# Performance work log

Hardware: AMD Instinct MI355X
Metric: run time of the kernel (lower is better)

Reference implementation:

```python
import jax, jax.numpy as jnp
import numpy as np

N, E = 40000, 640000          # nodes, edges (avg degree 16)
IN_N, IN_E = 8 + 768, 2       # in_dim_node + in_dim_text, in_dim_edge
H, OUT, NC, L = 128, 128, 5, 2
EPS_BN, EPS_DEN = 1e-5, 1e-6


def setup_inputs() -> dict:
    key = jax.random.key(0)
    ks = jax.random.split(key, 16)
    w = lambda k, shape: jax.random.normal(k, shape, jnp.float32) * 0.05
    return {
        "node_feat": jax.random.normal(ks[0], (N, IN_N), jnp.float32),
        "edge_feat": jax.random.normal(ks[1], (E, IN_E), jnp.float32),
        "src": jax.random.randint(ks[2], (E,), 0, N),
        "dst": jax.random.randint(ks[3], (E,), 0, N),
        "enc_nw": w(ks[4], (IN_N, H)), "enc_nb": jnp.zeros((H,), jnp.float32),
        "enc_ew": w(ks[5], (IN_E, H)), "enc_eb": jnp.zeros((H,), jnp.float32),
        # per layer: 5 linears (order A, B, C, D, E)
        "lin_w": w(ks[6], (L, 5, H, H)), "lin_b": jnp.zeros((L, 5, H), jnp.float32),
        "bnh_g": jnp.ones((L, H), jnp.float32), "bnh_b": jnp.zeros((L, H), jnp.float32),
        "bne_g": jnp.ones((L, H), jnp.float32), "bne_b": jnp.zeros((L, H), jnp.float32),
        "mlp_w1": w(ks[7], (H, OUT)), "mlp_b1": jnp.zeros((OUT,), jnp.float32),
        "mlp_w2": w(ks[8], (OUT, NC)), "mlp_b2": jnp.zeros((NC,), jnp.float32),
    }


def _bn(x, g, b):
    # training-mode BatchNorm1d: batch stats, biased variance, eps=1e-5
    m = jnp.mean(x, axis=0)
    v = jnp.var(x, axis=0)
    return (x - m) * jax.lax.rsqrt(v + EPS_BN) * g + b


def reference(node_feat, edge_feat, src, dst, enc_nw, enc_nb, enc_ew, enc_eb,
              lin_w, lin_b, bnh_g, bnh_b, bne_g, bne_b,
              mlp_w1, mlp_b1, mlp_w2, mlp_b2):
    n = node_feat.shape[0]
    h = node_feat @ enc_nw + enc_nb          # [N, H]
    e = edge_feat @ enc_ew + enc_eb          # [E, H]
    for l in range(L):
        Ah = h @ lin_w[l, 0] + lin_b[l, 0]
        Bh = h @ lin_w[l, 1] + lin_b[l, 1]
        Ce = e @ lin_w[l, 2] + lin_b[l, 2]
        Dh = h @ lin_w[l, 3] + lin_b[l, 3]
        Eh = h @ lin_w[l, 4] + lin_b[l, 4]
        e_new = Ce + Dh[src] + Eh[dst]       # [E, H] edge gate logits
        sigma = jax.nn.sigmoid(e_new)
        num = jax.ops.segment_sum(sigma * Bh[src], dst, num_segments=n)
        den = jax.ops.segment_sum(sigma, dst, num_segments=n)
        h_new = Ah + num / (den + EPS_DEN)
        h = jax.nn.relu(_bn(h_new, bnh_g[l], bnh_b[l]))
        e = jax.nn.relu(_bn(e_new, bne_g[l], bne_b[l]))
    # MLP readout per node (dropout p=0 -> identity)
    logits = jax.nn.relu(h @ mlp_w1 + mlp_b1) @ mlp_w2 + mlp_b2
    return logits
```

## Files before the change

kernel.cpp:

```cpp
#include <hip/hip_runtime.h>
#include <math.h>

#define NN 40000
#define NE 640000
#define KIN 776
#define HH 128
#define NCLS 5

typedef __attribute__((ext_vector_type(8))) short bf16x8;
typedef __attribute__((ext_vector_type(4))) short bf16x4;
typedef __attribute__((ext_vector_type(4))) float f32x4;

__device__ __forceinline__ float bf2f(short u) {
    return __uint_as_float(((unsigned)(unsigned short)u) << 16);
}
__device__ __forceinline__ short f2bf(float f) {
    unsigned u = __float_as_uint(f);
    u += 0x7fffu + ((u >> 16) & 1u);
    return (short)(u >> 16);
}

enum { A_F32 = 0 };

template<int NSTEP, bool TAIL8>
__global__ __launch_bounds__(256)
void mfma_gemm(const float* __restrict__ Af, const short* __restrict__ Wp,
               const float* __restrict__ bias, short* __restrict__ Cb, int K)
{
    const int lane = threadIdx.x & 63;
    const int wave = threadIdx.x >> 6;
    const int q = lane >> 4;
    const int c16 = lane & 15;
    const int row = blockIdx.x * 64 + wave * 16 + c16;

    f32x4 acc[8];
#pragma unroll
    for (int n = 0; n < 8; ++n) acc[n] = (f32x4){0.f, 0.f, 0.f, 0.f};

    for (int kt = 0; kt < NSTEP; ++kt) {
        bf16x8 afrag;
        const int kbase = kt * 32 + q * 8;
        if (!TAIL8 || kt < NSTEP - 1 || q == 0) {
            const float* p = Af + (size_t)row * K + kbase;
            const float4 x = *(const float4*)p;
            const float4 y = *(const float4*)(p + 4);
            afrag[0] = f2bf(x.x); afrag[1] = f2bf(x.y);
            afrag[2] = f2bf(x.z); afrag[3] = f2bf(x.w);
            afrag[4] = f2bf(y.x); afrag[5] = f2bf(y.y);
            afrag[6] = f2bf(y.z); afrag[7] = f2bf(y.w);
        } else {
#pragma unroll
            for (int j = 0; j < 8; ++j) afrag[j] = 0;
        }
        const int kb = kt * 4 + q;
#pragma unroll
        for (int n = 0; n < 8; ++n) {
            const bf16x8 wfrag =
                *(const bf16x8*)(Wp + (size_t)kb * 1024 + (n * 16 + c16) * 8);
            acc[n] = __builtin_amdgcn_mfma_f32_16x16x32_bf16(wfrag, afrag, acc[n], 0, 0, 0);
        }
    }
#pragma unroll
    for (int n = 0; n < 8; ++n) {
        const int col = n * 16 + q * 4;
        const float4 b4 = *(const float4*)(bias + col);
        bf16x4 o;
        o[0] = f2bf(acc[n][0] + b4.x); o[1] = f2bf(acc[n][1] + b4.y);
        o[2] = f2bf(acc[n][2] + b4.z); o[3] = f2bf(acc[n][3] + b4.w);
        *(bf16x4*)(Cb + (size_t)row * HH + col) = o;
    }
}

__global__ __launch_bounds__(256)
void edge2_k(short* __restrict__ enew, const short* __restrict__ Wp,
             const float* __restrict__ bias, const float* __restrict__ bnp,
             const short* __restrict__ Dh, const short* __restrict__ Eh,
             const int* __restrict__ src_s, const int* __restrict__ dst_s)
{
    const int lane = threadIdx.x & 63;
    const int wave = threadIdx.x >> 6;
    const int q = lane >> 4;
    const int c16 = lane & 15;
    const int row0 = blockIdx.x * 128 + wave * 16 + c16;
    const int row1 = row0 + 64;

    const int s0 = src_s[row0], d0 = dst_s[row0];
    const int s1 = src_s[row1], d1 = dst_s[row1];

    f32x4 acc[2][8];
#pragma unroll
    for (int n = 0; n < 8; ++n) {
        const int col = n * 16 + q * 4;
        const float4 b4 = *(const float4*)(bias + col);
        const bf16x4 dh0 = *(const bf16x4*)(Dh + (size_t)s0 * HH + col);
        const bf16x4 eh0 = *(const bf16x4*)(Eh + (size_t)d0 * HH + col);
        const bf16x4 dh1 = *(const bf16x4*)(Dh + (size_t)s1 * HH + col);
        const bf16x4 eh1 = *(const bf16x4*)(Eh + (size_t)d1 * HH + col);
        const float bb[4] = {b4.x, b4.y, b4.z, b4.w};
#pragma unroll
        for (int j = 0; j < 4; ++j) {
            acc[0][n][j] = bb[j] + bf2f(dh0[j]) + bf2f(eh0[j]);
            acc[1][n][j] = bb[j] + bf2f(dh1[j]) + bf2f(eh1[j]);
        }
    }

#pragma unroll
    for (int kt = 0; kt < 4; ++kt) {
        const int kbase = kt * 32 + q * 8;
        const float4 sc0 = *(const float4*)(bnp + kbase);
        const float4 sc1 = *(const float4*)(bnp + kbase + 4);
        const float4 sh0 = *(const float4*)(bnp + HH + kbase);
        const float4 sh1 = *(const float4*)(bnp + HH + kbase + 4);
        const float scv[8] = {sc0.x, sc0.y, sc0.z, sc0.w, sc1.x, sc1.y, sc1.z, sc1.w};
        const float shv[8] = {sh0.x, sh0.y, sh0.z, sh0.w, sh1.x, sh1.y, sh1.z, sh1.w};
        const bf16x8 r0 = *(const bf16x8*)(enew + (size_t)row0 * HH + kbase);
        const bf16x8 r1 = *(const bf16x8*)(enew + (size_t)row1 * HH + kbase);
        bf16x8 a0, a1;
#pragma unroll
        for (int j = 0; j < 8; ++j) {
            a0[j] = f2bf(fmaxf(fmaf(bf2f(r0[j]), scv[j], shv[j]), 0.f));
            a1[j] = f2bf(fmaxf(fmaf(bf2f(r1[j]), scv[j], shv[j]), 0.f));
        }
        const int kb = kt * 4 + q;
#pragma unroll
        for (int n = 0; n < 8; ++n) {
            const bf16x8 wfrag =
                *(const bf16x8*)(Wp + (size_t)kb * 1024 + (n * 16 + c16) * 8);
            acc[0][n] = __builtin_amdgcn_mfma_f32_16x16x32_bf16(wfrag, a0, acc[0][n], 0, 0, 0);
            acc[1][n] = __builtin_amdgcn_mfma_f32_16x16x32_bf16(wfrag, a1, acc[1][n], 0, 0, 0);
        }
    }

#pragma unroll
    for (int n = 0; n < 8; ++n) {
        const int col = n * 16 + q * 4;
        bf16x4 o0, o1;
#pragma unroll
        for (int j = 0; j < 4; ++j) {
            o0[j] = f2bf(acc[0][n][j]);
            o1[j] = f2bf(acc[1][n][j]);
        }
        *(bf16x4*)(enew + (size_t)row0 * HH + col) = o0;
        *(bf16x4*)(enew + (size_t)row1 * HH + col) = o1;
    }
}

template<bool ABN>
__global__ __launch_bounds__(256, 2)
void fused4_k(const short* __restrict__ hb, const float* __restrict__ hf,
              const float* __restrict__ bnp,
              const short* __restrict__ w0, const short* __restrict__ w1,
              const short* __restrict__ w2, const short* __restrict__ w3,
              const float* __restrict__ b0, const float* __restrict__ b1,
              const float* __restrict__ b2, const float* __restrict__ b3,
              float* __restrict__ Ah, short* __restrict__ Bh,
              short* __restrict__ Dh, short* __restrict__ Eh)
{
    const int lane = threadIdx.x & 63;
    const int wave = threadIdx.x >> 6;
    const int q = lane >> 4;
    const int c16 = lane & 15;
    const int row = blockIdx.x * 64 + wave * 16 + c16;

    f32x4 acc[4][8];
#pragma unroll
    for (int t = 0; t < 4; ++t)
#pragma unroll
        for (int n = 0; n < 8; ++n) acc[t][n] = (f32x4){0.f, 0.f, 0.f, 0.f};

    const short* const ws[4] = {w0, w1, w2, w3};
#pragma unroll
    for (int kt = 0; kt < 4; ++kt) {
        const int kbase = kt * 32 + q * 8;
        bf16x8 afrag;
        if (!ABN) {
            afrag = *(const bf16x8*)(hb + (size_t)row * HH + kbase);
        } else {
            const float* p = hf + (size_t)row * HH + kbase;
            const float4 x = *(const float4*)p;
            const float4 y = *(const float4*)(p + 4);
            const float4 s0 = *(const float4*)(bnp + kbase);
            const float4 s1 = *(const float4*)(bnp + kbase + 4);
            const float4 t0 = *(const float4*)(bnp + HH + kbase);
            const float4 t1 = *(const float4*)(bnp + HH + kbase + 4);
            const float xv[8] = {x.x, x.y, x.z, x.w, y.x, y.y, y.z, y.w};
            const float scv[8] = {s0.x, s0.y, s0.z, s0.w, s1.x, s1.y, s1.z, s1.w};
            const float shv[8] = {t0.x, t0.y, t0.z, t0.w, t1.x, t1.y, t1.z, t1.w};
#pragma unroll
            for (int j = 0; j < 8; ++j)
                afrag[j] = f2bf(fmaxf(fmaf(xv[j], scv[j], shv[j]), 0.f));
        }
        const int kb = kt * 4 + q;
#pragma unroll
        for (int t = 0; t < 4; ++t)
#pragma unroll
            for (int n = 0; n < 8; ++n) {
                const bf16x8 wfrag =
                    *(const bf16x8*)(ws[t] + (size_t)kb * 1024 + (n * 16 + c16) * 8);
                acc[t][n] = __builtin_amdgcn_mfma_f32_16x16x32_bf16(wfrag, afrag, acc[t][n], 0, 0, 0);
            }
    }

    const float* const bs[4] = {b0, b1, b2, b3};
#pragma unroll
    for (int t = 0; t < 4; ++t) {
#pragma unroll
        for (int n = 0; n < 8; ++n) {
            const int col = n * 16 + q * 4;
            const float4 b4 = *(const float4*)(bs[t] + col);
            const float v[4] = {acc[t][n][0] + b4.x, acc[t][n][1] + b4.y,
                                acc[t][n][2] + b4.z, acc[t][n][3] + b4.w};
            if (t == 0) {
                *(float4*)(Ah + (size_t)row * HH + col) = make_float4(v[0], v[1], v[2], v[3]);
            } else {
                bf16x4 o;
#pragma unroll
                for (int j = 0; j < 4; ++j) o[j] = f2bf(v[j]);
                short* dstp = (t == 1) ? Bh : ((t == 2) ? Dh : Eh);
                *(bf16x4*)(dstp + (size_t)row * HH + col) = o;
            }
        }
    }
}

__global__ __launch_bounds__(256)
void readout_k(const float* __restrict__ hnew, const float* __restrict__ bnp,
               const short* __restrict__ Wp, const float* __restrict__ b1,
               const float* __restrict__ w2, const float* __restrict__ b2,
               float* __restrict__ out)
{
    const int lane = threadIdx.x & 63;
    const int wave = threadIdx.x >> 6;
    const int q = lane >> 4;
    const int c16 = lane & 15;
    const int row = blockIdx.x * 64 + wave * 16 + c16;

    f32x4 acc[8];
#pragma unroll
    for (int n = 0; n < 8; ++n) acc[n] = (f32x4){0.f, 0.f, 0.f, 0.f};

#pragma unroll
    for (int kt = 0; kt < 4; ++kt) {
        const int kbase = kt * 32 + q * 8;
        const float* p = hnew + (size_t)row * HH + kbase;
        const float4 x = *(const float4*)p;
        const float4 y = *(const float4*)(p + 4);
        const float4 s0 = *(const float4*)(bnp + kbase);
        const float4 s1 = *(const float4*)(bnp + kbase + 4);
        const float4 t0 = *(const float4*)(bnp + HH + kbase);
        const float4 t1 = *(const float4*)(bnp + HH + kbase + 4);
        const float xv[8] = {x.x, x.y, x.z, x.w, y.x, y.y, y.z, y.w};
        const float scv[8] = {s0.x, s0.y, s0.z, s0.w, s1.x, s1.y, s1.z, s1.w};
        const float shv[8] = {t0.x, t0.y, t0.z, t0.w, t1.x, t1.y, t1.z, t1.w};
        bf16x8 afrag;
#pragma unroll
        for (int j = 0; j < 8; ++j)
            afrag[j] = f2bf(fmaxf(fmaf(xv[j], scv[j], shv[j]), 0.f));
        const int kb = kt * 4 + q;
#pragma unroll
        for (int n = 0; n < 8; ++n) {
            const bf16x8 wfrag =
                *(const bf16x8*)(Wp + (size_t)kb * 1024 + (n * 16 + c16) * 8);
            acc[n] = __builtin_amdgcn_mfma_f32_16x16x32_bf16(wfrag, afrag, acc[n], 0, 0, 0);
        }
    }

    float part[NCLS] = {};
#pragma unroll
    for (int n = 0; n < 8; ++n) {
        const int col = n * 16 + q * 4;
        const float4 b4 = *(const float4*)(b1 + col);
        const float bb[4] = {b4.x, b4.y, b4.z, b4.w};
#pragma unroll
        for (int j = 0; j < 4; ++j) {
            const float zv = fmaxf(acc[n][j] + bb[j], 0.f);
#pragma unroll
            for (int t = 0; t < NCLS; ++t)
                part[t] = fmaf(zv, w2[(col + j) * NCLS + t], part[t]);
        }
    }
#pragma unroll
    for (int t = 0; t < NCLS; ++t) {
        part[t] += __shfl_xor(part[t], 16, 64);
        part[t] += __shfl_xor(part[t], 32, 64);
    }
    if (q == 0) {
#pragma unroll
        for (int t = 0; t < NCLS; ++t)
            out[(size_t)row * NCLS + t] = part[t] + b2[t];
    }
}

__global__ __launch_bounds__(256)
void prepack_k(const float* __restrict__ enc_nw, const float* __restrict__ lin_w,
               const float* __restrict__ mlp_w1, short* __restrict__ wp)
{
    const int t = blockIdx.x * 256 + threadIdx.x;
    if (t >= 260 * 128) return;
    const int kbg = t >> 7, col = t & 127;
    const int kb0[11]  = {0, 100, 116, 132, 148, 164, 180, 196, 212, 228, 244};
    const int psel[11] = {0, 1, 1, 1, 1, 1, 1, 1, 1, 1, 2};
    const int soff[11] = {0, 0 * 16384, 1 * 16384, 3 * 16384, 4 * 16384,
                          5 * 16384, 6 * 16384, 7 * 16384, 8 * 16384, 9 * 16384, 0};
    const int Ksrc[11] = {KIN, 128, 128, 128, 128, 128, 128, 128, 128, 128, 128};
    int e = 10;
    while (e > 0 && kbg < kb0[e]) --e;
    const float* base = (psel[e] == 0) ? enc_nw : ((psel[e] == 1) ? lin_w : mlp_w1);
    const int kbl = kbg - kb0[e];
    bf16x8 o;
#pragma unroll
    for (int j = 0; j < 8; ++j) {
        const int k = kbl * 8 + j;
        const float v = (k < Ksrc[e]) ? base[(size_t)soff[e] + (size_t)k * HH + col] : 0.f;
        o[j] = f2bf(v);
    }
    *(bf16x8*)(wp + (size_t)kbg * 1024 + col * 8) = o;
}

__global__ void gpre_k(const float* __restrict__ enc_ew, const float* __restrict__ enc_eb,
                       const float* __restrict__ Wc, const float* __restrict__ bc,
                       float* __restrict__ G)
{
    const int c = threadIdx.x;
    float a0 = 0.f, a1 = 0.f, ab = 0.f;
    for (int k = 0; k < HH; ++k) {
        const float w = Wc[k * HH + c];
        a0 = fmaf(enc_ew[k], w, a0);
        a1 = fmaf(enc_ew[HH + k], w, a1);
        ab = fmaf(enc_eb[k], w, ab);
    }
    G[c] = a0; G[HH + c] = a1; G[2 * HH + c] = ab + bc[c];
}

__global__ __launch_bounds__(256)
void edge1_k(const float* __restrict__ ef, const int* __restrict__ eidx,
             const int* __restrict__ src_s, const int* __restrict__ dst_s,
             const float* __restrict__ G,
             const short* __restrict__ Dh, const short* __restrict__ Eh,
             short* __restrict__ enew, float* __restrict__ pbuf)
{
    const int tid = threadIdx.x;
    const int er = tid >> 4, cg = tid & 15;
    const int col = cg * 8;
    const float4 g00 = *(const float4*)(G + col);
    const float4 g01 = *(const float4*)(G + col + 4);
    const float4 g10 = *(const float4*)(G + HH + col);
    const float4 g11 = *(const float4*)(G + HH + col + 4);
    const float4 gb0 = *(const float4*)(G + 2 * HH + col);
    const float4 gb1 = *(const float4*)(G + 2 * HH + col + 4);
    const float G0v[8] = {g00.x, g00.y, g00.z, g00.w, g01.x, g01.y, g01.z, g01.w};
    const float G1v[8] = {g10.x, g10.y, g10.z, g10.w, g11.x, g11.y, g11.z, g11.w};
    const float GBv[8] = {gb0.x, gb0.y, gb0.z, gb0.w, gb1.x, gb1.y, gb1.z, gb1.w};
    float sa[8] = {}, qa[8] = {};
    for (int it = 0; it < 16; ++it) {
        const int i = blockIdx.x * 256 + it * 16 + er;
        const int e = eidx[i];
        const float f0 = ef[(size_t)e * 2];
        const float f1 = ef[(size_t)e * 2 + 1];
        const int s = src_s[i], d = dst_s[i];
        const bf16x8 dh = *(const bf16x8*)(Dh + (size_t)s * HH + col);
        const bf16x8 eh = *(const bf16x8*)(Eh + (size_t)d * HH + col);
        bf16x8 o;
#pragma unroll
        for (int j = 0; j < 8; ++j) {
            const float v = fmaf(f0, G0v[j], fmaf(f1, G1v[j], GBv[j]))
                            + bf2f(dh[j]) + bf2f(eh[j]);
            sa[j] += v; qa[j] += v * v;
            o[j] = f2bf(v);
        }
        *(bf16x8*)(enew + (size_t)i * HH + col) = o;
    }
    __shared__ float sred[16][136];
    const int slot = (blockIdx.x & 63) * 256;
#pragma unroll
    for (int j = 0; j < 8; ++j) sred[er][col + j] = sa[j];
    __syncthreads();
    for (int s2 = 8; s2 > 0; s2 >>= 1) {
        if (er < s2)
#pragma unroll
            for (int j = 0; j < 8; ++j) sred[er][col + j] += sred[er + s2][col + j];
        __syncthreads();
    }
    if (er == 0)
#pragma unroll
        for (int j = 0; j < 8; ++j) atomicAdd(pbuf + slot + col + j, sred[0][col + j]);
    __syncthreads();
#pragma unroll
    for (int j = 0; j < 8; ++j) sred[er][col + j] = qa[j];
    __syncthreads();
    for (int s2 = 8; s2 > 0; s2 >>= 1) {
        if (er < s2)
#pragma unroll
            for (int j = 0; j < 8; ++j) sred[er][col + j] += sred[er + s2][col + j];
        __syncthreads();
    }
    if (er == 0)
#pragma unroll
        for (int j = 0; j < 8; ++j) atomicAdd(pbuf + slot + 128 + col + j, sred[0][col + j]);
}

__global__ __launch_bounds__(256)
void hist_k(const int* __restrict__ dst, int* __restrict__ cnt)
{
    const int e = blockIdx.x * 256 + threadIdx.x;
    if (e < NE) atomicAdd(cnt + dst[e], 1);
}

__global__ __launch_bounds__(1024)
void scan_k(const int* __restrict__ cnt, int* __restrict__ rowptr, int* __restrict__ wr)
{
    __shared__ int s[1024];
    const int t = threadIdx.x;
    const int base = t * 40;
    int sum = 0;
    for (int i = 0; i < 40; ++i) {
        const int idx = base + i;
        if (idx < NN) sum += cnt[idx];
    }
    s[t] = sum;
    __syncthreads();
    for (int off = 1; off < 1024; off <<= 1) {
        const int v = (t >= off) ? s[t - off] : 0;
        __syncthreads();
        s[t] += v;
        __syncthreads();
    }
    int run = (t == 0) ? 0 : s[t - 1];
    for (int i = 0; i < 40; ++i) {
        const int idx = base + i;
        if (idx < NN) {
            rowptr[idx] = run;
            wr[idx] = run;
            run += cnt[idx];
        }
    }
    if (t == 1023) rowptr[NN] = s[1023];
}

__global__ __launch_bounds__(256)
void scatter_k2(const int* __restrict__ dst, const int* __restrict__ src,
                int* __restrict__ wr, int* __restrict__ eidx,
                int* __restrict__ src_s, int* __restrict__ dst_s)
{
    const int e = blockIdx.x * 256 + threadIdx.x;
    if (e < NE) {
        const int d = dst[e];
        const int p = atomicAdd(wr + d, 1);
        eidx[p] = e;
        src_s[p] = src[e];
        dst_s[p] = d;
    }
}

__global__ __launch_bounds__(256)
void seg_reduce_v(const short* __restrict__ enew, const int* __restrict__ rowptr,
                  const int* __restrict__ src_s, const short* __restrict__ Bh,
                  const float* __restrict__ Ah, float* __restrict__ hnew,
                  float* __restrict__ pbuf)
{
    const int wv = threadIdx.x >> 6;
    const int lane = threadIdx.x & 63;
    const int slot = lane >> 4;
    const int cg = lane & 15;
    const int col = cg * 8;
    const int n0 = (blockIdx.x * 4 + wv) * 8;
    float sa[8] = {}, qa[8] = {};
    for (int nn = 0; nn < 8; ++nn) {
        const int n = n0 + nn;
        const int k0 = rowptr[n], k1 = rowptr[n + 1];
        float num[8] = {}, den[8] = {};
        for (int k = k0 + slot; k < k1; k += 4) {
            const bf16x8 ev = *(const bf16x8*)(enew + (size_t)k * HH + col);
            const int s = src_s[k];
            const bf16x8 bv = *(const bf16x8*)(Bh + (size_t)s * HH + col);
#pragma unroll
            for (int j = 0; j < 8; ++j) {
                const float sg = 1.f / (1.f + __expf(-bf2f(ev[j])));
                den[j] += sg;
                num[j] = fmaf(sg, bf2f(bv[j]), num[j]);
            }
        }
#pragma unroll
        for (int j = 0; j < 8; ++j) {
            num[j] += __shfl_xor(num[j], 16, 64);
            den[j] += __shfl_xor(den[j], 16, 64);
            num[j] += __shfl_xor(num[j], 32, 64);
            den[j] += __shfl_xor(den[j], 32, 64);
        }
        if (slot == 0) {
            const size_t idx = (size_t)n * HH + col;
            const float4 a0 = *(const float4*)(Ah + idx);
            const float4 a1 = *(const float4*)(Ah + idx + 4);
            const float av[8] = {a0.x, a0.y, a0.z, a0.w, a1.x, a1.y, a1.z, a1.w};
            float x[8];
#pragma unroll
            for (int j = 0; j < 8; ++j) {
                x[j] = av[j] + num[j] / (den[j] + 1e-6f);
                sa[j] += x[j]; qa[j] += x[j] * x[j];
            }
            *(float4*)(hnew + idx) = make_float4(x[0], x[1], x[2], x[3]);
            *(float4*)(hnew + idx + 4) = make_float4(x[4], x[5], x[6], x[7]);
        }
    }
    if (slot == 0) {
        const int sl = (blockIdx.x & 63) * 256;
#pragma unroll
        for (int j = 0; j < 8; ++j) {
            atomicAdd(pbuf + sl + col + j, sa[j]);
            atomicAdd(pbuf + sl + 128 + col + j, qa[j]);
        }
    }
}

__global__ void make_bnp2(const float* __restrict__ pbuf, const float* __restrict__ g,
                          const float* __restrict__ b, float cntInv,
                          float* __restrict__ out)
{
    const int c = threadIdx.x;
    float s = 0.f, q = 0.f;
    for (int i = 0; i < 64; ++i) {
        s += pbuf[i * 256 + c];
        q += pbuf[i * 256 + 128 + c];
    }
    const float m = s * cntInv;
    const float var = q * cntInv - m * m;
    const float rs = rsqrtf(var + 1e-5f);
    const float sc = g[c] * rs;
    out[c] = sc;
    out[128 + c] = b[c] - m * sc;
}

extern "C" void kernel_launch(void* const* d_in, const int* in_sizes, int n_in,
                              void* d_out, int out_size, void* d_ws, size_t ws_size,
                              hipStream_t stream)
{
    const float* node_feat = (const float*)d_in[0];
    const float* edge_feat = (const float*)d_in[1];
    const int*   src       = (const int*)d_in[2];
    const int*   dst       = (const int*)d_in[3];
    const float* enc_nw    = (const float*)d_in[4];
    const float* enc_nb    = (const float*)d_in[5];
    const float* enc_ew    = (const float*)d_in[6];
    const float* enc_eb    = (const float*)d_in[7];
    const float* lin_w     = (const float*)d_in[8];
    const float* lin_b     = (const float*)d_in[9];
    const float* bnh_g     = (const float*)d_in[10];
    const float* bnh_b     = (const float*)d_in[11];
    const float* bne_g     = (const float*)d_in[12];
    const float* bne_b     = (const float*)d_in[13];
    const float* mlp_w1    = (const float*)d_in[14];
    const float* mlp_b1    = (const float*)d_in[15];
    const float* mlp_w2    = (const float*)d_in[16];
    const float* mlp_b2    = (const float*)d_in[17];
    float* out = (float*)d_out;

    char* base = (char*)d_ws;
    size_t off = 0;
    auto alloc = [&](size_t bytes) -> void* {
        void* p = base + off;
        off = (off + bytes + 255) & ~(size_t)255;
        return p;
    };
    const size_t NH = (size_t)NN * HH;
    float* hnew  = (float*)alloc(NH * 4);
    float* Ah    = (float*)alloc(NH * 4);
    short* h0    = (short*)alloc(NH * 2);
    short* Bh    = (short*)alloc(NH * 2);
    short* Dh    = (short*)alloc(NH * 2);
    short* Eh    = (short*)alloc(NH * 2);
    short* enew  = (short*)alloc((size_t)NE * HH * 2);
    short* wpack = (short*)alloc((size_t)260 * 1024 * 2);
    float* G     = (float*)alloc(384 * 4);
    float* bnpe  = (float*)alloc(256 * 4);
    float* bnph  = (float*)alloc(256 * 4);
    float* pbe   = (float*)alloc(16384 * 4);
    float* pbh0  = (float*)alloc(16384 * 4);
    float* pbh1  = (float*)alloc(16384 * 4);
    int* cnt     = (int*)alloc(NN * 4);
    int* rowptr  = (int*)alloc((NN + 1) * 4);
    int* wr      = (int*)alloc(NN * 4);
    int* eidx    = (int*)alloc((size_t)NE * 4);
    int* src_s   = (int*)alloc((size_t)NE * 4);
    int* dst_s   = (int*)alloc((size_t)NE * 4);

    const dim3 blk(256);

    hipMemsetAsync(cnt, 0, NN * 4, stream);
    hipMemsetAsync(pbe, 0, 3 * 16384 * 4, stream);
    hist_k<<<2500, blk, 0, stream>>>(dst, cnt);
    scan_k<<<1, 1024, 0, stream>>>(cnt, rowptr, wr);
    scatter_k2<<<2500, blk, 0, stream>>>(dst, src, wr, eidx, src_s, dst_s);
    prepack_k<<<130, blk, 0, stream>>>(enc_nw, lin_w, mlp_w1, wpack);
    gpre_k<<<1, 128, 0, stream>>>(enc_ew, enc_eb, lin_w + 2 * 16384, lin_b + 2 * HH, G);

    mfma_gemm<25, true><<<625, blk, 0, stream>>>(node_feat, wpack, enc_nb, h0, KIN);

    {
        const float* Bv = lin_b;
        fused4_k<false><<<625, blk, 0, stream>>>(
            h0, nullptr, nullptr,
            wpack + (size_t)100 * 1024, wpack + (size_t)116 * 1024,
            wpack + (size_t)132 * 1024, wpack + (size_t)148 * 1024,
            Bv + 0 * HH, Bv + 1 * HH, Bv + 3 * HH, Bv + 4 * HH,
            Ah, Bh, Dh, Eh);
        edge1_k<<<2500, blk, 0, stream>>>(edge_feat, eidx, src_s, dst_s, G,
                                          Dh, Eh, enew, pbe);
        make_bnp2<<<1, 128, 0, stream>>>(pbe, bne_g, bne_b, 1.f / NE, bnpe);
        seg_reduce_v<<<1250, blk, 0, stream>>>(enew, rowptr, src_s, Bh, Ah, hnew, pbh0);
        make_bnp2<<<1, 128, 0, stream>>>(pbh0, bnh_g, bnh_b, 1.f / NN, bnph);
    }

    {
        const float* Bv = lin_b + 5 * HH;
        fused4_k<true><<<625, blk, 0, stream>>>(
            nullptr, hnew, bnph,
            wpack + (size_t)164 * 1024, wpack + (size_t)180 * 1024,
            wpack + (size_t)212 * 1024, wpack + (size_t)228 * 1024,
            Bv + 0 * HH, Bv + 1 * HH, Bv + 3 * HH, Bv + 4 * HH,
            Ah, Bh, Dh, Eh);
        edge2_k<<<5000, blk, 0, stream>>>(enew, wpack + (size_t)196 * 1024,
                                          Bv + 2 * HH, bnpe, Dh, Eh, src_s, dst_s);
        seg_reduce_v<<<1250, blk, 0, stream>>>(enew, rowptr, src_s, Bh, Ah, hnew, pbh1);
        make_bnp2<<<1, 128, 0, stream>>>(pbh1, bnh_g + HH, bnh_b + HH, 1.f / NN, bnph);
    }

    readout_k<<<625, blk, 0, stream>>>(hnew, bnph, wpack + (size_t)244 * 1024,
                                       mlp_b1, mlp_w2, mlp_b2, out);
}
```

Baseline: 816.0 us.

## Fuse layer-1 edge gating with segment reduce and recompute edge logits in layer 2

Layer-1 edge computation is merged into a per-destination segment reduction, so the [E,H] bf16 edge tensor is never written in layer 1. The layer-1 edge logits are recomputed inside the layer-2 edge kernel from edge features, a folded BN-scaled G matrix and the kept layer-0 Dh/Eh buffers. A separate small kernel computes the node BN statistics. This trades one large edge-tensor write and read for extra gathers and recomputation. It also needs extra Dh/Eh buffers so layer-1 values stay live.

```diff
diff --git a/kernel.cpp b/kernel.cpp
--- a/kernel.cpp
+++ b/kernel.cpp
@@ -19,8 +19,6 @@
     u += 0x7fffu + ((u >> 16) & 1u);
     return (short)(u >> 16);
 }
-
-enum { A_F32 = 0 };
 
 template<int NSTEP, bool TAIL8>
 __global__ __launch_bounds__(256)
@@ -68,80 +66,6 @@
         o[0] = f2bf(acc[n][0] + b4.x); o[1] = f2bf(acc[n][1] + b4.y);
         o[2] = f2bf(acc[n][2] + b4.z); o[3] = f2bf(acc[n][3] + b4.w);
         *(bf16x4*)(Cb + (size_t)row * HH + col) = o;
-    }
-}
-
-__global__ __launch_bounds__(256)
-void edge2_k(short* __restrict__ enew, const short* __restrict__ Wp,
-             const float* __restrict__ bias, const float* __restrict__ bnp,
-             const short* __restrict__ Dh, const short* __restrict__ Eh,
-             const int* __restrict__ src_s, const int* __restrict__ dst_s)
-{
-    const int lane = threadIdx.x & 63;
-    const int wave = threadIdx.x >> 6;
-    const int q = lane >> 4;
-    const int c16 = lane & 15;
-    const int row0 = blockIdx.x * 128 + wave * 16 + c16;
-    const int row1 = row0 + 64;
-
-    const int s0 = src_s[row0], d0 = dst_s[row0];
-    const int s1 = src_s[row1], d1 = dst_s[row1];
-
-    f32x4 acc[2][8];
-#pragma unroll
-    for (int n = 0; n < 8; ++n) {
-        const int col = n * 16 + q * 4;
-        const float4 b4 = *(const float4*)(bias + col);
-        const bf16x4 dh0 = *(const bf16x4*)(Dh + (size_t)s0 * HH + col);
-        const bf16x4 eh0 = *(const bf16x4*)(Eh + (size_t)d0 * HH + col);
-        const bf16x4 dh1 = *(const bf16x4*)(Dh + (size_t)s1 * HH + col);
-        const bf16x4 eh1 = *(const bf16x4*)(Eh + (size_t)d1 * HH + col);
-        const float bb[4] = {b4.x, b4.y, b4.z, b4.w};
-#pragma unroll
-        for (int j = 0; j < 4; ++j) {
-            acc[0][n][j] = bb[j] + bf2f(dh0[j]) + bf2f(eh0[j]);
-            acc[1][n][j] = bb[j] + bf2f(dh1[j]) + bf2f(eh1[j]);
-        }
-    }
-
-#pragma unroll
-    for (int kt = 0; kt < 4; ++kt) {
-        const int kbase = kt * 32 + q * 8;
-        const float4 sc0 = *(const float4*)(bnp + kbase);
-        const float4 sc1 = *(const float4*)(bnp + kbase + 4);
-        const float4 sh0 = *(const float4*)(bnp + HH + kbase);
-        const float4 sh1 = *(const float4*)(bnp + HH + kbase + 4);
-        const float scv[8] = {sc0.x, sc0.y, sc0.z, sc0.w, sc1.x, sc1.y, sc1.z, sc1.w};
-        const float shv[8] = {sh0.x, sh0.y, sh0.z, sh0.w, sh1.x, sh1.y, sh1.z, sh1.w};
-        const bf16x8 r0 = *(const bf16x8*)(enew + (size_t)row0 * HH + kbase);
-        const bf16x8 r1 = *(const bf16x8*)(enew + (size_t)row1 * HH + kbase);
-        bf16x8 a0, a1;
-#pragma unroll
-        for (int j = 0; j < 8; ++j) {
-            a0[j] = f2bf(fmaxf(fmaf(bf2f(r0[j]), scv[j], shv[j]), 0.f));
-            a1[j] = f2bf(fmaxf(fmaf(bf2f(r1[j]), scv[j], shv[j]), 0.f));
-        }
-        const int kb = kt * 4 + q;
-#pragma unroll
-        for (int n = 0; n < 8; ++n) {
-            const bf16x8 wfrag =
-                *(const bf16x8*)(Wp + (size_t)kb * 1024 + (n * 16 + c16) * 8);
-            acc[0][n] = __builtin_amdgcn_mfma_f32_16x16x32_bf16(wfrag, a0, acc[0][n], 0, 0, 0);
-            acc[1][n] = __builtin_amdgcn_mfma_f32_16x16x32_bf16(wfrag, a1, acc[1][n], 0, 0, 0);
-        }
-    }
-
-#pragma unroll
-    for (int n = 0; n < 8; ++n) {
-        const int col = n * 16 + q * 4;
-        bf16x4 o0, o1;
-#pragma unroll
-        for (int j = 0; j < 4; ++j) {
-            o0[j] = f2bf(acc[0][n][j]);
-            o1[j] = f2bf(acc[1][n][j]);
-        }
-        *(bf16x4*)(enew + (size_t)row0 * HH + col) = o0;
-        *(bf16x4*)(enew + (size_t)row1 * HH + col) = o1;
     }
 }
 
@@ -224,124 +148,20 @@
 }
 
 __global__ __launch_bounds__(256)
-void readout_k(const float* __restrict__ hnew, const float* __restrict__ bnp,
-               const short* __restrict__ Wp, const float* __restrict__ b1,
-               const float* __restrict__ w2, const float* __restrict__ b2,
-               float* __restrict__ out)
-{
+void edge1seg_k(const float* __restrict__ ef, const int* __restrict__ eidx,
+                const int* __restrict__ src_s, const int* __restrict__ rowptr,
+                const float* __restrict__ G,
+                const short* __restrict__ Dh, const short* __restrict__ Eh,
+                const short* __restrict__ Bh, const float* __restrict__ Ah,
+                float* __restrict__ hnew, float* __restrict__ pbuf)
+{
+    const int wv = threadIdx.x >> 6;
     const int lane = threadIdx.x & 63;
-    const int wave = threadIdx.x >> 6;
-    const int q = lane >> 4;
-    const int c16 = lane & 15;
-    const int row = blockIdx.x * 64 + wave * 16 + c16;
-
-    f32x4 acc[8];
-#pragma unroll
-    for (int n = 0; n < 8; ++n) acc[n] = (f32x4){0.f, 0.f, 0.f, 0.f};
-
-#pragma unroll
-    for (int kt = 0; kt < 4; ++kt) {
-        const int kbase = kt * 32 + q * 8;
-        const float* p = hnew + (size_t)row * HH + kbase;
-        const float4 x = *(const float4*)p;
-        const float4 y = *(const float4*)(p + 4);
-        const float4 s0 = *(const float4*)(bnp + kbase);
-        const float4 s1 = *(const float4*)(bnp + kbase + 4);
-        const float4 t0 = *(const float4*)(bnp + HH + kbase);
-        const float4 t1 = *(const float4*)(bnp + HH + kbase + 4);
-        const float xv[8] = {x.x, x.y, x.z, x.w, y.x, y.y, y.z, y.w};
-        const float scv[8] = {s0.x, s0.y, s0.z, s0.w, s1.x, s1.y, s1.z, s1.w};
-        const float shv[8] = {t0.x, t0.y, t0.z, t0.w, t1.x, t1.y, t1.z, t1.w};
-        bf16x8 afrag;
-#pragma unroll
-        for (int j = 0; j < 8; ++j)
-            afrag[j] = f2bf(fmaxf(fmaf(xv[j], scv[j], shv[j]), 0.f));
-        const int kb = kt * 4 + q;
-#pragma unroll
-        for (int n = 0; n < 8; ++n) {
-            const bf16x8 wfrag =
-                *(const bf16x8*)(Wp + (size_t)kb * 1024 + (n * 16 + c16) * 8);
-            acc[n] = __builtin_amdgcn_mfma_f32_16x16x32_bf16(wfrag, afrag, acc[n], 0, 0, 0);
-        }
-    }
-
-    float part[NCLS] = {};
-#pragma unroll
-    for (int n = 0; n < 8; ++n) {
-        const int col = n * 16 + q * 4;
-        const float4 b4 = *(const float4*)(b1 + col);
-        const float bb[4] = {b4.x, b4.y, b4.z, b4.w};
-#pragma unroll
-        for (int j = 0; j < 4; ++j) {
-            const float zv = fmaxf(acc[n][j] + bb[j], 0.f);
-#pragma unroll
-            for (int t = 0; t < NCLS; ++t)
-                part[t] = fmaf(zv, w2[(col + j) * NCLS + t], part[t]);
-        }
-    }
-#pragma unroll
-    for (int t = 0; t < NCLS; ++t) {
-        part[t] += __shfl_xor(part[t], 16, 64);
-        part[t] += __shfl_xor(part[t], 32, 64);
-    }
-    if (q == 0) {
-#pragma unroll
-        for (int t = 0; t < NCLS; ++t)
-            out[(size_t)row * NCLS + t] = part[t] + b2[t];
-    }
-}
-
-__global__ __launch_bounds__(256)
-void prepack_k(const float* __restrict__ enc_nw, const float* __restrict__ lin_w,
-               const float* __restrict__ mlp_w1, short* __restrict__ wp)
-{
-    const int t = blockIdx.x * 256 + threadIdx.x;
-    if (t >= 260 * 128) return;
-    const int kbg = t >> 7, col = t & 127;
-    const int kb0[11]  = {0, 100, 116, 132, 148, 164, 180, 196, 212, 228, 244};
-    const int psel[11] = {0, 1, 1, 1, 1, 1, 1, 1, 1, 1, 2};
-    const int soff[11] = {0, 0 * 16384, 1 * 16384, 3 * 16384, 4 * 16384,
-                          5 * 16384, 6 * 16384, 7 * 16384, 8 * 16384, 9 * 16384, 0};
-    const int Ksrc[11] = {KIN, 128, 128, 128, 128, 128, 128, 128, 128, 128, 128};
-    int e = 10;
-    while (e > 0 && kbg < kb0[e]) --e;
-    const float* base = (psel[e] == 0) ? enc_nw : ((psel[e] == 1) ? lin_w : mlp_w1);
-    const int kbl = kbg - kb0[e];
-    bf16x8 o;
-#pragma unroll
-    for (int j = 0; j < 8; ++j) {
-        const int k = kbl * 8 + j;
-        const float v = (k < Ksrc[e]) ? base[(size_t)soff[e] + (size_t)k * HH + col] : 0.f;
-        o[j] = f2bf(v);
-    }
-    *(bf16x8*)(wp + (size_t)kbg * 1024 + col * 8) = o;
-}
-
-__global__ void gpre_k(const float* __restrict__ enc_ew, const float* __restrict__ enc_eb,
-                       const float* __restrict__ Wc, const float* __restrict__ bc,
-                       float* __restrict__ G)
-{
-    const int c = threadIdx.x;
-    float a0 = 0.f, a1 = 0.f, ab = 0.f;
-    for (int k = 0; k < HH; ++k) {
-        const float w = Wc[k * HH + c];
-        a0 = fmaf(enc_ew[k], w, a0);
-        a1 = fmaf(enc_ew[HH + k], w, a1);
-        ab = fmaf(enc_eb[k], w, ab);
-    }
-    G[c] = a0; G[HH + c] = a1; G[2 * HH + c] = ab + bc[c];
-}
-
-__global__ __launch_bounds__(256)
-void edge1_k(const float* __restrict__ ef, const int* __restrict__ eidx,
-             const int* __restrict__ src_s, const int* __restrict__ dst_s,
-             const float* __restrict__ G,
-             const short* __restrict__ Dh, const short* __restrict__ Eh,
-             short* __restrict__ enew, float* __restrict__ pbuf)
-{
-    const int tid = threadIdx.x;
-    const int er = tid >> 4, cg = tid & 15;
+    const int slot = lane >> 4;
+    const int cg = lane & 15;
     const int col = cg * 8;
+    const int n0 = (blockIdx.x * 4 + wv) * 8;
+
     const float4 g00 = *(const float4*)(G + col);
     const float4 g01 = *(const float4*)(G + col + 4);
     const float4 g10 = *(const float4*)(G + HH + col);
@@ -351,29 +171,59 @@
     const float G0v[8] = {g00.x, g00.y, g00.z, g00.w, g01.x, g01.y, g01.z, g01.w};
     const float G1v[8] = {g10.x, g10.y, g10.z, g10.w, g11.x, g11.y, g11.z, g11.w};
     const float GBv[8] = {gb0.x, gb0.y, gb0.z, gb0.w, gb1.x, gb1.y, gb1.z, gb1.w};
-    float sa[8] = {}, qa[8] = {};
-    for (int it = 0; it < 16; ++it) {
-        const int i = blockIdx.x * 256 + it * 16 + er;
-        const int e = eidx[i];
-        const float f0 = ef[(size_t)e * 2];
-        const float f1 = ef[(size_t)e * 2 + 1];
-        const int s = src_s[i], d = dst_s[i];
-        const bf16x8 dh = *(const bf16x8*)(Dh + (size_t)s * HH + col);
-        const bf16x8 eh = *(const bf16x8*)(Eh + (size_t)d * HH + col);
-        bf16x8 o;
+
+    float esa[8] = {}, esq[8] = {};
+
+    for (int nn = 0; nn < 8; ++nn) {
+        const int n = n0 + nn;
+        const int k0 = rowptr[n], k1 = rowptr[n + 1];
+        const bf16x8 ehn = *(const bf16x8*)(Eh + (size_t)n * HH + col);
+        float ehv[8];
+#pragma unroll
+        for (int j = 0; j < 8; ++j) ehv[j] = bf2f(ehn[j]);
+        float num[8] = {}, den[8] = {};
+        for (int k = k0 + slot; k < k1; k += 4) {
+            const int e = eidx[k];
+            const int s = src_s[k];
+            const float f0 = ef[(size_t)e * 2];
+            const float f1 = ef[(size_t)e * 2 + 1];
+            const bf16x8 dh = *(const bf16x8*)(Dh + (size_t)s * HH + col);
+            const bf16x8 bh = *(const bf16x8*)(Bh + (size_t)s * HH + col);
+#pragma unroll
+            for (int j = 0; j < 8; ++j) {
+                const float v = fmaf(f0, G0v[j], fmaf(f1, G1v[j], GBv[j]))
+                                + bf2f(dh[j]) + ehv[j];
+                esa[j] += v; esq[j] += v * v;
+                const float sg = 1.f / (1.f + __expf(-v));
+                den[j] += sg;
+                num[j] = fmaf(sg, bf2f(bh[j]), num[j]);
+            }
+        }
 #pragma unroll
         for (int j = 0; j < 8; ++j) {
-            const float v = fmaf(f0, G0v[j], fmaf(f1, G1v[j], GBv[j]))
-                            + bf2f(dh[j]) + bf2f(eh[j]);
-            sa[j] += v; qa[j] += v * v;
-            o[j] = f2bf(v);
-        }
-        *(bf16x8*)(enew + (size_t)i * HH + col) = o;
-    }
+            num[j] += __shfl_xor(num[j], 16, 64);
+            den[j] += __shfl_xor(den[j], 16, 64);
+            num[j] += __shfl_xor(num[j], 32, 64);
+            den[j] += __shfl_xor(den[j], 32, 64);
+        }
+        if (slot == 0) {
+            const size_t idx = (size_t)n * HH + col;
+            const float4 a0 = *(const float4*)(Ah + idx);
+            const float4 a1 = *(const float4*)(Ah + idx + 4);
+            const float av[8] = {a0.x, a0.y, a0.z, a0.w, a1.x, a1.y, a1.z, a1.w};
+            float x[8];
+#pragma unroll
+            for (int j = 0; j < 8; ++j) x[j] = av[j] + num[j] / (den[j] + 1e-6f);
+            *(float4*)(hnew + idx) = make_float4(x[0], x[1], x[2], x[3]);
+            *(float4*)(hnew + idx + 4) = make_float4(x[4], x[5], x[6], x[7]);
+        }
+    }
+
     __shared__ float sred[16][136];
-    const int slot = (blockIdx.x & 63) * 256;
-#pragma unroll
-    for (int j = 0; j < 8; ++j) sred[er][col + j] = sa[j];
+    const int er = threadIdx.x >> 4;
+    const int slotp = (blockIdx.x & 63) * 256;
+#pragma unroll
+    for (int j = 0; j < 8; ++j) sred[er][col + j] = esa[j];
     __syncthreads();
     for (int s2 = 8; s2 > 0; s2 >>= 1) {
         if (er < s2)
@@ -383,10 +233,10 @@
     }
     if (er == 0)
 #pragma unroll
-        for (int j = 0; j < 8; ++j) atomicAdd(pbuf + slot + col + j, sred[0][col + j]);
+        for (int j = 0; j < 8; ++j) atomicAdd(pbuf + slotp + col + j, sred[0][col + j]);
     __syncthreads();
 #pragma unroll
-    for (int j = 0; j < 8; ++j) sred[er][col + j] = qa[j];
+    for (int j = 0; j < 8; ++j) sred[er][col + j] = esq[j];
     __syncthreads();
     for (int s2 = 8; s2 > 0; s2 >>= 1) {
         if (er < s2)
@@ -396,59 +246,109 @@
     }
     if (er == 0)
 #pragma unroll
-        for (int j = 0; j < 8; ++j) atomicAdd(pbuf + slot + 128 + col + j, sred[0][col + j]);
-}
-
-__global__ __launch_bounds__(256)
-void hist_k(const int* __restrict__ dst, int* __restrict__ cnt)
-{
-    const int e = blockIdx.x * 256 + threadIdx.x;
-    if (e < NE) atomicAdd(cnt + dst[e], 1);
-}
-
-__global__ __launch_bounds__(1024)
-void scan_k(const int* __restrict__ cnt, int* __restrict__ rowptr, int* __restrict__ wr)
-{
-    __shared__ int s[1024];
-    const int t = threadIdx.x;
-    const int base = t * 40;
-    int sum = 0;
-    for (int i = 0; i < 40; ++i) {
-        const int idx = base + i;
-        if (idx < NN) sum += cnt[idx];
-    }
-    s[t] = sum;
-    __syncthreads();
-    for (int off = 1; off < 1024; off <<= 1) {
-        const int v = (t >= off) ? s[t - off] : 0;
-        __syncthreads();
-        s[t] += v;
-        __syncthreads();
-    }
-    int run = (t == 0) ? 0 : s[t - 1];
-    for (int i = 0; i < 40; ++i) {
-        const int idx = base + i;
-        if (idx < NN) {
-            rowptr[idx] = run;
-            wr[idx] = run;
-            run += cnt[idx];
-        }
-    }
-    if (t == 1023) rowptr[NN] = s[1023];
-}
-
-__global__ __launch_bounds__(256)
-void scatter_k2(const int* __restrict__ dst, const int* __restrict__ src,
-                int* __restrict__ wr, int* __restrict__ eidx,
-                int* __restrict__ src_s, int* __restrict__ dst_s)
-{
-    const int e = blockIdx.x * 256 + threadIdx.x;
-    if (e < NE) {
-        const int d = dst[e];
-        const int p = atomicAdd(wr + d, 1);
-        eidx[p] = e;
-        src_s[p] = src[e];
-        dst_s[p] = d;
+        for (int j = 0; j < 8; ++j) atomicAdd(pbuf + slotp + 128 + col + j, sred[0][col + j]);
+}
+
+__global__ void gm_k(const float* __restrict__ G, const float* __restrict__ bnpe,
+                     float* __restrict__ Gm)
+{
+    const int c = threadIdx.x;
+    const float sc = bnpe[c], sh = bnpe[128 + c];
+    Gm[c] = G[c] * sc;
+    Gm[128 + c] = G[HH + c] * sc;
+    Gm[256 + c] = fmaf(G[2 * HH + c], sc, sh);
+    Gm[384 + c] = sc;
+}
+
+__global__ __launch_bounds__(256)
+void edge2_k(const int* __restrict__ eidx, const float* __restrict__ ef,
+             const float* __restrict__ Gm,
+             const short* __restrict__ Dh0, const short* __restrict__ Eh0,
+             const short* __restrict__ Dh1, const short* __restrict__ Eh1,
+             const int* __restrict__ src_s, const int* __restrict__ dst_s,
+             const short* __restrict__ Wp, const float* __restrict__ bias,
+             short* __restrict__ enew)
+{
+    const int lane = threadIdx.x & 63;
+    const int wave = threadIdx.x >> 6;
+    const int q = lane >> 4;
+    const int c16 = lane & 15;
+    const int row0 = blockIdx.x * 128 + wave * 16 + c16;
+    const int row1 = row0 + 64;
+
+    const int s0 = src_s[row0], d0 = dst_s[row0];
+    const int s1 = src_s[row1], d1 = dst_s[row1];
+    const int e0 = eidx[row0], e1 = eidx[row1];
+    const float2 ef0 = *(const float2*)(ef + (size_t)e0 * 2);
+    const float2 ef1 = *(const float2*)(ef + (size_t)e1 * 2);
+
+    f32x4 acc[2][8];
+#pragma unroll
+    for (int n = 0; n < 8; ++n) {
+        const int col = n * 16 + q * 4;
+        const float4 b4 = *(const float4*)(bias + col);
+        const bf16x4 dh0 = *(const bf16x4*)(Dh1 + (size_t)s0 * HH + col);
+        const bf16x4 eh0 = *(const bf16x4*)(Eh1 + (size_t)d0 * HH + col);
+        const bf16x4 dh1 = *(const bf16x4*)(Dh1 + (size_t)s1 * HH + col);
+        const bf16x4 eh1 = *(const bf16x4*)(Eh1 + (size_t)d1 * HH + col);
+        const float bb[4] = {b4.x, b4.y, b4.z, b4.w};
+#pragma unroll
+        for (int j = 0; j < 4; ++j) {
+            acc[0][n][j] = bb[j] + bf2f(dh0[j]) + bf2f(eh0[j]);
+            acc[1][n][j] = bb[j] + bf2f(dh1[j]) + bf2f(eh1[j]);
+        }
+    }
+
+#pragma unroll
+    for (int kt = 0; kt < 4; ++kt) {
+        const int kbase = kt * 32 + q * 8;
+        const float4 p0 = *(const float4*)(Gm + kbase);
+        const float4 p1 = *(const float4*)(Gm + kbase + 4);
+        const float4 p2 = *(const float4*)(Gm + 128 + kbase);
+        const float4 p3 = *(const float4*)(Gm + 128 + kbase + 4);
+        const float4 p4 = *(const float4*)(Gm + 256 + kbase);
+        const float4 p5 = *(const float4*)(Gm + 256 + kbase + 4);
+        const float4 p6 = *(const float4*)(Gm + 384 + kbase);
+        const float4 p7 = *(const float4*)(Gm + 384 + kbase + 4);
+        const float g0s[8] = {p0.x, p0.y, p0.z, p0.w, p1.x, p1.y, p1.z, p1.w};
+        const float g1s[8] = {p2.x, p2.y, p2.z, p2.w, p3.x, p3.y, p3.z, p3.w};
+        const float gbs[8] = {p4.x, p4.y, p4.z, p4.w, p5.x, p5.y, p5.z, p5.w};
+        const float scv[8] = {p6.x, p6.y, p6.z, p6.w, p7.x, p7.y, p7.z, p7.w};
+        const bf16x8 dA0 = *(const bf16x8*)(Dh0 + (size_t)s0 * HH + kbase);
+        const bf16x8 eA0 = *(const bf16x8*)(Eh0 + (size_t)d0 * HH + kbase);
+        const bf16x8 dA1 = *(const bf16x8*)(Dh0 + (size_t)s1 * HH + kbase);
+        const bf16x8 eA1 = *(const bf16x8*)(Eh0 + (size_t)d1 * HH + kbase);
+        bf16x8 a0, a1;
+#pragma unroll
+        for (int j = 0; j < 8; ++j) {
+            float t0 = fmaf(scv[j], bf2f(dA0[j]) + bf2f(eA0[j]), gbs[j]);
+            t0 = fmaf(ef0.x, g0s[j], fmaf(ef0.y, g1s[j], t0));
+            a0[j] = f2bf(fmaxf(t0, 0.f));
+            float t1 = fmaf(scv[j], bf2f(dA1[j]) + bf2f(eA1[j]), gbs[j]);
+            t1 = fmaf(ef1.x, g0s[j], fmaf(ef1.y, g1s[j], t1));
+            a1[j] = f2bf(fmaxf(t1, 0.f));
+        }
+        const int kb = kt * 4 + q;
+#pragma unroll
+        for (int n = 0; n < 8; ++n) {
+            const bf16x8 wfrag =
+                *(const bf16x8*)(Wp + (size_t)kb * 1024 + (n * 16 + c16) * 8);
+            acc[0][n] = __builtin_amdgcn_mfma_f32_16x16x32_bf16(wfrag, a0, acc[0][n], 0, 0, 0);
+            acc[1][n] = __builtin_amdgcn_mfma_f32_16x16x32_bf16(wfrag, a1, acc[1][n], 0, 0, 0);
+        }
+    }
+
+#pragma unroll
+    for (int n = 0; n < 8; ++n) {
+        const int col = n * 16 + q * 4;
+        bf16x4 o0, o1;
+#pragma unroll
+        for (int j = 0; j < 4; ++j) {
+            o0[j] = f2bf(acc[0][n][j]);
+            o1[j] = f2bf(acc[1][n][j]);
+        }
+        *(bf16x4*)(enew + (size_t)row0 * HH + col) = o0;
+        *(bf16x4*)(enew + (size_t)row1 * HH + col) = o1;
     }
 }
 
@@ -510,6 +410,189 @@
             atomicAdd(pbuf + sl + 128 + col + j, qa[j]);
         }
     }
+}
+
+__global__ __launch_bounds__(256)
+void readout_k(const float* __restrict__ hnew, const float* __restrict__ bnp,
+               const short* __restrict__ Wp, const float* __restrict__ b1,
+               const float* __restrict__ w2, const float* __restrict__ b2,
+               float* __restrict__ out)
+{
+    const int lane = threadIdx.x & 63;
+    const int wave = threadIdx.x >> 6;
+    const int q = lane >> 4;
+    const int c16 = lane & 15;
+    const int row = blockIdx.x * 64 + wave * 16 + c16;
+
+    f32x4 acc[8];
+#pragma unroll
+    for (int n = 0; n < 8; ++n) acc[n] = (f32x4){0.f, 0.f, 0.f, 0.f};
+
+#pragma unroll
+    for (int kt = 0; kt < 4; ++kt) {
+        const int kbase = kt * 32 + q * 8;
+        const float* p = hnew + (size_t)row * HH + kbase;
+        const float4 x = *(const float4*)p;
+        const float4 y = *(const float4*)(p + 4);
+        const float4 s0 = *(const float4*)(bnp + kbase);
+        const float4 s1 = *(const float4*)(bnp + kbase + 4);
+        const float4 t0 = *(const float4*)(bnp + HH + kbase);
+        const float4 t1 = *(const float4*)(bnp + HH + kbase + 4);
+        const float xv[8] = {x.x, x.y, x.z, x.w, y.x, y.y, y.z, y.w};
+        const float scv[8] = {s0.x, s0.y, s0.z, s0.w, s1.x, s1.y, s1.z, s1.w};
+        const float shv[8] = {t0.x, t0.y, t0.z, t0.w, t1.x, t1.y, t1.z, t1.w};
+        bf16x8 afrag;
+#pragma unroll
+        for (int j = 0; j < 8; ++j)
+            afrag[j] = f2bf(fmaxf(fmaf(xv[j], scv[j], shv[j]), 0.f));
+        const int kb = kt * 4 + q;
+#pragma unroll
+        for (int n = 0; n < 8; ++n) {
+            const bf16x8 wfrag =
+                *(const bf16x8*)(Wp + (size_t)kb * 1024 + (n * 16 + c16) * 8);
+            acc[n] = __builtin_amdgcn_mfma_f32_16x16x32_bf16(wfrag, afrag, acc[n], 0, 0, 0);
+        }
+    }
+
+    float part[NCLS] = {};
+#pragma unroll
+    for (int n = 0; n < 8; ++n) {
+        const int col = n * 16 + q * 4;
+        const float4 b4 = *(const float4*)(b1 + col);
+        const float bb[4] = {b4.x, b4.y, b4.z, b4.w};
+#pragma unroll
+        for (int j = 0; j < 4; ++j) {
+            const float zv = fmaxf(acc[n][j] + bb[j], 0.f);
+#pragma unroll
+            for (int t = 0; t < NCLS; ++t)
+                part[t] = fmaf(zv, w2[(col + j) * NCLS + t], part[t]);
+        }
+    }
+#pragma unroll
+    for (int t = 0; t < NCLS; ++t) {
+        part[t] += __shfl_xor(part[t], 16, 64);
+        part[t] += __shfl_xor(part[t], 32, 64);
+    }
+    if (q == 0) {
+#pragma unroll
+        for (int t = 0; t < NCLS; ++t)
+            out[(size_t)row * NCLS + t] = part[t] + b2[t];
+    }
+}
+
+__global__ __launch_bounds__(256)
+void prepack_k(const float* __restrict__ enc_nw, const float* __restrict__ lin_w,
+               const float* __restrict__ mlp_w1, short* __restrict__ wp)
+{
+    const int t = blockIdx.x * 256 + threadIdx.x;
+    if (t >= 260 * 128) return;
+    const int kbg = t >> 7, col = t & 127;
+    const int kb0[11]  = {0, 100, 116, 132, 148, 164, 180, 196, 212, 228, 244};
+    const int psel[11] = {0, 1, 1, 1, 1, 1, 1, 1, 1, 1, 2};
+    const int soff[11] = {0, 0 * 16384, 1 * 16384, 3 * 16384, 4 * 16384,
+                          5 * 16384, 6 * 16384, 7 * 16384, 8 * 16384, 9 * 16384, 0};
+    const int Ksrc[11] = {KIN, 128, 128, 128, 128, 128, 128, 128, 128, 128, 128};
+    int e = 10;
+    while (e > 0 && kbg < kb0[e]) --e;
+    const float* base = (psel[e] == 0) ? enc_nw : ((psel[e] == 1) ? lin_w : mlp_w1);
+    const int kbl = kbg - kb0[e];
+    bf16x8 o;
+#pragma unroll
+    for (int j = 0; j < 8; ++j) {
+        const int k = kbl * 8 + j;
+        const float v = (k < Ksrc[e]) ? base[(size_t)soff[e] + (size_t)k * HH + col] : 0.f;
+        o[j] = f2bf(v);
+    }
+    *(bf16x8*)(wp + (size_t)kbg * 1024 + col * 8) = o;
+}
+
+__global__ void gpre_k(const float* __restrict__ enc_ew, const float* __restrict__ enc_eb,
+                       const float* __restrict__ Wc, const float* __restrict__ bc,
+                       float* __restrict__ G)
+{
+    const int c = threadIdx.x;
+    float a0 = 0.f, a1 = 0.f, ab = 0.f;
+    for (int k = 0; k < HH; ++k) {
+        const float w = Wc[k * HH + c];
+        a0 = fmaf(enc_ew[k], w, a0);
+        a1 = fmaf(enc_ew[HH + k], w, a1);
+        ab = fmaf(enc_eb[k], w, ab);
+    }
+    G[c] = a0; G[HH + c] = a1; G[2 * HH + c] = ab + bc[c];
+}
+
+__global__ __launch_bounds__(256)
+void hist_k(const int* __restrict__ dst, int* __restrict__ cnt)
+{
+    const int e = blockIdx.x * 256 + threadIdx.x;
+    if (e < NE) atomicAdd(cnt + dst[e], 1);
+}
+
+__global__ __launch_bounds__(1024)
+void scan_k(const int* __restrict__ cnt, int* __restrict__ rowptr, int* __restrict__ wr)
+{
+    __shared__ int s[1024];
+    const int t = threadIdx.x;
+    const int base = t * 40;
+    int sum = 0;
+    for (int i = 0; i < 40; ++i) {
+        const int idx = base + i;
+        if (idx < NN) sum += cnt[idx];
+    }
+    s[t] = sum;
+    __syncthreads();
+    for (int off = 1; off < 1024; off <<= 1) {
+        const int v = (t >= off) ? s[t - off] : 0;
+        __syncthreads();
+        s[t] += v;
+        __syncthreads();
+    }
+    int run = (t == 0) ? 0 : s[t - 1];
+    for (int i = 0; i < 40; ++i) {
+        const int idx = base + i;
+        if (idx < NN) {
+            rowptr[idx] = run;
+            wr[idx] = run;
+            run += cnt[idx];
+        }
+    }
+    if (t == 1023) rowptr[NN] = s[1023];
+}
+
+__global__ __launch_bounds__(256)
+void scatter_k(const int* __restrict__ dst, const int* __restrict__ src,
+               int* __restrict__ wr, int* __restrict__ eidx,
+               int* __restrict__ src_s, int* __restrict__ dst_s)
+{
+    const int e = blockIdx.x * 256 + threadIdx.x;
+    if (e < NE) {
+        const int d = dst[e];
+        const int p = atomicAdd(wr + d, 1);
+        eidx[p] = e;
+        src_s[p] = src[e];
+        dst_s[p] = d;
+    }
+}
+
+__global__ __launch_bounds__(256)
+void hstats_k(const float* __restrict__ hnew, float* __restrict__ pbuf)
+{
+    const int tid = threadIdx.x;
+    const int c = tid & 127, sub = tid >> 7;
+    const int r0 = blockIdx.x * 256;
+    float sa = 0.f, qa = 0.f;
+    for (int i = sub; i < 256; i += 2) {
+        const int r = r0 + i;
+        if (r >= NN) break;
+        const float x = hnew[(size_t)r * HH + c];
+        sa += x; qa += x * x;
+    }
+    __shared__ float red[256];
+    red[tid] = sa; __syncthreads();
+    if (tid < 128) atomicAdd(pbuf + (blockIdx.x & 63) * 256 + c, red[tid] + red[tid + 128]);
+    __syncthreads();
+    red[tid] = qa; __syncthreads();
+    if (tid < 128) atomicAdd(pbuf + (blockIdx.x & 63) * 256 + 128 + c, red[tid] + red[tid + 128]);
 }
 
 __global__ void make_bnp2(const float* __restrict__ pbuf, const float* __restrict__ g,
@@ -565,12 +648,15 @@
     float* hnew  = (float*)alloc(NH * 4);
     float* Ah    = (float*)alloc(NH * 4);
     short* h0    = (short*)alloc(NH * 2);
-    short* Bh    = (short*)alloc(NH * 2);
-    short* Dh    = (short*)alloc(NH * 2);
-    short* Eh    = (short*)alloc(NH * 2);
+    short* Bh0   = (short*)alloc(NH * 2);
+    short* Dh0   = (short*)alloc(NH * 2);
+    short* Eh0   = (short*)alloc(NH * 2);
+    short* Dh1   = (short*)alloc(NH * 2);
+    short* Eh1   = (short*)alloc(NH * 2);
     short* enew  = (short*)alloc((size_t)NE * HH * 2);
     short* wpack = (short*)alloc((size_t)260 * 1024 * 2);
     float* G     = (float*)alloc(384 * 4);
+    float* Gm    = (float*)alloc(512 * 4);
     float* bnpe  = (float*)alloc(256 * 4);
     float* bnph  = (float*)alloc(256 * 4);
     float* pbe   = (float*)alloc(16384 * 4);
@@ -589,7 +675,7 @@
     hipMemsetAsync(pbe, 0, 3 * 16384 * 4, stream);
     hist_k<<<2500, blk, 0, stream>>>(dst, cnt);
     scan_k<<<1, 1024, 0, stream>>>(cnt, rowptr, wr);
-    scatter_k2<<<2500, blk, 0, stream>>>(dst, src, wr, eidx, src_s, dst_s);
+    scatter_k<<<2500, blk, 0, stream>>>(dst, src, wr, eidx, src_s, dst_s);
     prepack_k<<<130, blk, 0, stream>>>(enc_nw, lin_w, mlp_w1, wpack);
     gpre_k<<<1, 128, 0, stream>>>(enc_ew, enc_eb, lin_w + 2 * 16384, lin_b + 2 * HH, G);
 
@@ -602,25 +688,28 @@
             wpack + (size_t)100 * 1024, wpack + (size_t)116 * 1024,
             wpack + (size_t)132 * 1024, wpack + (size_t)148 * 1024,
             Bv + 0 * HH, Bv + 1 * HH, Bv + 3 * HH, Bv + 4 * HH,
-            Ah, Bh, Dh, Eh);
-        edge1_k<<<2500, blk, 0, stream>>>(edge_feat, eidx, src_s, dst_s, G,
-                                          Dh, Eh, enew, pbe);
+            Ah, Bh0, Dh0, Eh0);
+        edge1seg_k<<<1250, blk, 0, stream>>>(edge_feat, eidx, src_s, rowptr, G,
+                                             Dh0, Eh0, Bh0, Ah, hnew, pbe);
         make_bnp2<<<1, 128, 0, stream>>>(pbe, bne_g, bne_b, 1.f / NE, bnpe);
-        seg_reduce_v<<<1250, blk, 0, stream>>>(enew, rowptr, src_s, Bh, Ah, hnew, pbh0);
+        gm_k<<<1, 128, 0, stream>>>(G, bnpe, Gm);
+        hstats_k<<<157, blk, 0, stream>>>(hnew, pbh0);
         make_bnp2<<<1, 128, 0, stream>>>(pbh0, bnh_g, bnh_b, 1.f / NN, bnph);
     }
 
     {
         const float* Bv = lin_b + 5 * HH;
+        short* Bh1 = h0;
         fused4_k<true><<<625, blk, 0, stream>>>(
             nullptr, hnew, bnph,
             wpack + (size_t)164 * 1024, wpack + (size_t)180 * 1024,
             wpack + (size_t)212 * 1024, wpack + (size_t)228 * 1024,
             Bv + 0 * HH, Bv + 1 * HH, Bv + 3 * HH, Bv + 4 * HH,
-            Ah, Bh, Dh, Eh);
-        edge2_k<<<5000, blk, 0, stream>>>(enew, wpack + (size_t)196 * 1024,
-                                          Bv + 2 * HH, bnpe, Dh, Eh, src_s, dst_s);
-        seg_reduce_v<<<1250, blk, 0, stream>>>(enew, rowptr, src_s, Bh, Ah, hnew, pbh1);
+            Ah, Bh1, Dh1, Eh1);
+        edge2_k<<<5000, blk, 0, stream>>>(eidx, edge_feat, Gm, Dh0, Eh0, Dh1, Eh1,
+                                          src_s, dst_s, wpack + (size_t)196 * 1024,
+                                          Bv + 2 * HH, enew);
+        seg_reduce_v<<<1250, blk, 0, stream>>>(enew, rowptr, src_s, Bh1, Ah, hnew, pbh1);
         make_bnp2<<<1, 128, 0, stream>>>(pbh1, bnh_g + HH, bnh_b + HH, 1.f / NN, bnph);
     }
 
```

After: 854.7 us. 4.7% more time.
